# Kernel tuning notes

Measured on AMD Instinct MI355X. Metric: run time of the kernel, lower is better.

The kernel has to match this reference:

```python
import jax, jax.numpy as jnp
import numpy as np

EMBED_DIM = 1024
NUM_HEADS = 16
HEAD_DIM = EMBED_DIM // NUM_HEADS
EPSILON = 0.01
C = 2.0 + EPSILON
SCORE_SCALE = 1.0
B, L = 2, 2048


def setup_inputs() -> dict:
    key = jax.random.key(0)
    k0, k1, k2, k3, k4 = jax.random.split(key, 5)
    x = jax.random.normal(k0, (B, L, EMBED_DIM), dtype=jnp.float32)
    # flax Linear kernels: (in, out)
    W_qkv = jax.random.normal(k1, (EMBED_DIM, 3 * EMBED_DIM), dtype=jnp.float32) / np.sqrt(EMBED_DIM)
    b_qkv = jnp.zeros((3 * EMBED_DIM,), dtype=jnp.float32)
    W_out = jax.random.normal(k2, (EMBED_DIM, EMBED_DIM), dtype=jnp.float32) / np.sqrt(EMBED_DIM)
    b_out = jnp.zeros((EMBED_DIM,), dtype=jnp.float32)
    return {"x": x, "W_qkv": W_qkv, "b_qkv": b_qkv, "W_out": W_out, "b_out": b_out}


def reference(x, W_qkv, b_qkv, W_out, b_out):
    Bb, Ll, E = x.shape
    qkv = x @ W_qkv + b_qkv                      # [B, L, 3E]
    q, k, v = jnp.split(qkv, 3, axis=-1)
    def to_heads(t):
        return t.reshape(Bb, Ll, NUM_HEADS, HEAD_DIM).transpose(0, 2, 1, 3)  # [B,H,L,D]
    q, k, v = to_heads(q), to_heads(k), to_heads(v)
    q_norm = q / jnp.linalg.norm(q, axis=-1, keepdims=True)
    k_norm = k / jnp.linalg.norm(k, axis=-1, keepdims=True)
    x_dot = jnp.einsum('bhid,bhjd->bhij', q_norm, k_norm)   # [B,H,L,L]
    scores = (x_dot ** 2) / (C - 2.0 * x_dot) * SCORE_SCALE
    mask = jnp.triu(jnp.ones((Ll, Ll), dtype=scores.dtype), k=1) * -1e9
    scores = scores + mask[None, None, :, :]
    attn = jax.nn.softmax(scores, axis=-1)
    out = jnp.einsum('bhij,bhjd->bhid', attn, v)            # [B,H,L,D]
    out = out.transpose(0, 2, 1, 3).reshape(Bb, Ll, E)
    return out @ W_out + b_out
```

## Files before the change

kernel.cpp:

```cpp
#include <hip/hip_runtime.h>
#include <cstdint>
#include <cstddef>

#define B_DIM 2
#define L_DIM 2048
#define E_DIM 1024
#define H_DIM 16
#define HD    64
#define M_ROWS (B_DIM * L_DIM)
#define QKV_N  (3 * E_DIM)
#define C_CONST 2.01f
#define NCH_BH 40
#define LOG2E 1.4426950408889634f
#define LN2   0.6931471805599453f

typedef unsigned short ushort_t;
typedef __attribute__((ext_vector_type(8))) short bf16x8;
typedef __attribute__((ext_vector_type(4))) float f32x4;

__device__ __forceinline__ unsigned int f2bf(float f) {
    union { float f; unsigned int u; } v; v.f = f;
    return (v.u + 0x7FFFu + ((v.u >> 16) & 1u)) >> 16;
}
__device__ __forceinline__ float bf2f_lo(unsigned int u) {
    union { unsigned int u; float f; } v; v.u = u << 16; return v.f;
}
__device__ __forceinline__ float bf2f_hi(unsigned int u) {
    union { unsigned int u; float f; } v; v.u = u & 0xffff0000u; return v.f;
}

__device__ __forceinline__ void gload16(const void* g, void* l) {
    __builtin_amdgcn_global_load_lds(
        (const __attribute__((address_space(1))) void*)g,
        (__attribute__((address_space(3))) void*)l, 16, 0, 0);
}

__device__ __forceinline__ void transpose_tile_dev(
    const float* __restrict__ in, ushort_t* __restrict__ out,
    int R, int Cn, int c0, int r0, int tid, float t[64][65])
{
    for (int idx = tid; idx < 4096; idx += 256) {
        const int r = idx >> 6, c = idx & 63;
        t[r][c] = in[(size_t)(r0 + r) * Cn + c0 + c];
    }
    __syncthreads();
    for (int idx = tid; idx < 4096; idx += 256) {
        const int c = idx >> 6, r = idx & 63;
        out[(size_t)(c0 + c) * R + r0 + r] = (ushort_t)f2bf(t[r][c]);
    }
}

__global__ __launch_bounds__(256) void prep_kernel(
    const float* __restrict__ x, ushort_t* __restrict__ xb,
    const float* __restrict__ Wqkv, ushort_t* __restrict__ WqkvT,
    const float* __restrict__ Wout, ushort_t* __restrict__ WoutT)
{
    __shared__ float t[64][65];
    const int bx = blockIdx.x;
    const int tid = threadIdx.x;
    if (bx < 4096) {
        const int i = bx * 256 + tid;
        const float4 v = ((const float4*)x)[i];
        uint2 p;
        p.x = f2bf(v.x) | (f2bf(v.y) << 16);
        p.y = f2bf(v.z) | (f2bf(v.w) << 16);
        ((uint2*)xb)[i] = p;
    } else if (bx < 4096 + 768) {
        const int idx = bx - 4096;
        transpose_tile_dev(Wqkv, WqkvT, E_DIM, QKV_N, (idx % 48) * 64, (idx / 48) * 64, tid, t);
    } else {
        const int idx = bx - 4864;
        transpose_tile_dev(Wout, WoutT, E_DIM, E_DIM, (idx & 15) * 64, (idx >> 4) * 64, tid, t);
    }
}

template<int NCOLS, int MODE>
__global__ __launch_bounds__(256) void gemm_bt_kernel(
    const ushort_t* __restrict__ A, const ushort_t* __restrict__ BT,
    const float* __restrict__ bias, float* __restrict__ outf,
    ushort_t* __restrict__ q16, ushort_t* __restrict__ k16,
    ushort_t* __restrict__ vt16)
{
    __shared__ __align__(16) ushort_t Abuf[2][128 * 32];
    __shared__ __align__(16) ushort_t Bbuf[2][128 * 32];
    const int tid = threadIdx.x;
    const int wave = tid >> 6, lane = tid & 63;
    const int m0 = blockIdx.x * 128, n0 = blockIdx.y * 128;
    const int wr = (wave >> 1) * 64, wc = (wave & 1) * 64;
    const int g = lane >> 4, l15 = lane & 15;

    f32x4 acc[4][4];
    #pragma unroll
    for (int i = 0; i < 4; ++i)
        #pragma unroll
        for (int j = 0; j < 4; ++j) acc[i][j] = f32x4{0.f, 0.f, 0.f, 0.f};

    const int sr = tid >> 2;
    const int sc = (tid & 3) * 8;
    const ushort_t* Asrc0 = A + (size_t)(m0 + sr) * 1024 + sc;
    const ushort_t* Asrc1 = A + (size_t)(m0 + 64 + sr) * 1024 + sc;
    const ushort_t* Bsrc0 = BT + (size_t)(n0 + sr) * 1024 + sc;
    const ushort_t* Bsrc1 = BT + (size_t)(n0 + 64 + sr) * 1024 + sc;

    gload16(Asrc0, &Abuf[0][tid * 8]);
    gload16(Asrc1, &Abuf[0][2048 + tid * 8]);
    gload16(Bsrc0, &Bbuf[0][tid * 8]);
    gload16(Bsrc1, &Bbuf[0][2048 + tid * 8]);
    __syncthreads();

    for (int k0 = 0; k0 < 1024; k0 += 32) {
        const int cur = (k0 >> 5) & 1;
        if (k0 + 32 < 1024) {
            gload16(Asrc0 + k0 + 32, &Abuf[cur ^ 1][tid * 8]);
            gload16(Asrc1 + k0 + 32, &Abuf[cur ^ 1][2048 + tid * 8]);
            gload16(Bsrc0 + k0 + 32, &Bbuf[cur ^ 1][tid * 8]);
            gload16(Bsrc1 + k0 + 32, &Bbuf[cur ^ 1][2048 + tid * 8]);
        }

        bf16x8 af[4];
        #pragma unroll
        for (int mt = 0; mt < 4; ++mt)
            af[mt] = *(const bf16x8*)&Abuf[cur][(wr + mt * 16 + l15) * 32 + 8 * g];
        #pragma unroll
        for (int nt = 0; nt < 4; ++nt) {
            const bf16x8 bfr = *(const bf16x8*)&Bbuf[cur][(wc + nt * 16 + l15) * 32 + 8 * g];
            #pragma unroll
            for (int mt = 0; mt < 4; ++mt)
                acc[mt][nt] = __builtin_amdgcn_mfma_f32_16x16x32_bf16(af[mt], bfr, acc[mt][nt], 0, 0, 0);
        }
        __syncthreads();
    }

    if (MODE == 0) {
        const int nBase = n0 + wc;
        const int sel = nBase >> 10;
        const int h   = (nBase & 1023) >> 6;
        float bv[4];
        #pragma unroll
        for (int nt = 0; nt < 4; ++nt) bv[nt] = bias[nBase + nt * 16 + l15];

        if (sel <= 1) {
            ushort_t* dst16 = (sel == 0) ? q16 : k16;
            #pragma unroll
            for (int mt = 0; mt < 4; ++mt) {
                float val[4][4], ss[4] = {0.f, 0.f, 0.f, 0.f};
                #pragma unroll
                for (int nt = 0; nt < 4; ++nt)
                    #pragma unroll
                    for (int r = 0; r < 4; ++r) {
                        const float v = acc[mt][nt][r] + bv[nt];
                        val[nt][r] = v;
                        ss[r] = fmaf(v, v, ss[r]);
                    }
                #pragma unroll
                for (int r = 0; r < 4; ++r) {
                    float t = ss[r];
                    t += __shfl_xor(t, 1); t += __shfl_xor(t, 2);
                    t += __shfl_xor(t, 4); t += __shfl_xor(t, 8);
                    ss[r] = 1.0f / sqrtf(t);
                }
                #pragma unroll
                for (int r = 0; r < 4; ++r) {
                    const int m = m0 + wr + mt * 16 + 4 * g + r;
                    const int bb = m >> 11, ll = m & 2047;
                    ushort_t* base = dst16 + ((size_t)((bb * H_DIM + h) * L_DIM + ll)) * HD + l15;
                    #pragma unroll
                    for (int nt = 0; nt < 4; ++nt)
                        base[nt * 16] = (ushort_t)f2bf(val[nt][r] * ss[r]);
                }
            }
        } else {
            const int bb = m0 >> 11;
            #pragma unroll
            for (int nt = 0; nt < 4; ++nt) {
                const int d = nt * 16 + l15;
                ushort_t* vbase = vt16 + ((size_t)((bb * H_DIM + h) * HD + d)) * L_DIM;
                #pragma unroll
                for (int mt = 0; mt < 4; ++mt) {
                    const int key = (m0 & 2047) + wr + mt * 16 + 4 * g;
                    const float v0 = acc[mt][nt][0] + bv[nt];
                    const float v1 = acc[mt][nt][1] + bv[nt];
                    const float v2 = acc[mt][nt][2] + bv[nt];
                    const float v3 = acc[mt][nt][3] + bv[nt];
                    uint2 pk;
                    asm("v_cvt_pk_bf16_f32 %0, %1, %2" : "=v"(pk.x) : "v"(v0), "v"(v1));
                    asm("v_cvt_pk_bf16_f32 %0, %1, %2" : "=v"(pk.y) : "v"(v2), "v"(v3));
                    *(uint2*)&vbase[key] = pk;
                }
            }
        }
    } else {
        #pragma unroll
        for (int nt = 0; nt < 4; ++nt) {
            const int n = n0 + wc + nt * 16 + l15;
            const float bvv = bias[n];
            #pragma unroll
            for (int mt = 0; mt < 4; ++mt)
                #pragma unroll
                for (int r = 0; r < 4; ++r) {
                    const int m = m0 + wr + mt * 16 + 4 * g + r;
                    outf[(size_t)m * E_DIM + n] = acc[mt][nt][r] + bvv;
                }
        }
    }
}

__global__ __launch_bounds__(512) void attn_mfma_kernel(
    const ushort_t* __restrict__ qn, const ushort_t* __restrict__ kn,
    const ushort_t* __restrict__ vt,
    ushort_t* __restrict__ pO, float* __restrict__ pl, float* __restrict__ pm)
{
    __shared__ __align__(16) ushort_t Qs[128 * 64];
    __shared__ __align__(16) ushort_t Ks[2][64 * 64];
    __shared__ __align__(16) ushort_t Vs[2][64 * 64];

    int c = blockIdx.x, qtp = 0, s = 0;
    #pragma unroll
    for (int gg = 0; gg < 4; ++gg) {
        const int sz = 4 * (gg + 1);
        if (c < sz) { qtp = 4 * gg + c / (gg + 1); s = c - (c / (gg + 1)) * (gg + 1); break; }
        c -= sz;
    }
    const int bh = blockIdx.y;
    const int cid = bh * NCH_BH + blockIdx.x;
    const int q0 = qtp * 128;
    const int kt0 = 8 * s;
    const int ktEnd = min(8 * s + 8, 2 * qtp + 2);

    const int tid = threadIdx.x, w = tid >> 6, lane = tid & 63;
    const int g = lane >> 4, l15 = lane & 15;
    ushort_t* Pw = &Qs[w * 16 * 64];

    const ushort_t* Qg = qn + ((size_t)bh * L_DIM + q0) * HD;
    const ushort_t* Kg = kn + (size_t)bh * L_DIM * HD;
    const ushort_t* Vg = vt + (size_t)bh * HD * L_DIM;

    const int srow = tid >> 3, sch = tid & 7;
    const int qr2 = (tid + 512) >> 3, qc2 = (tid + 512) & 7;

    {
        const int j0 = kt0 * 64;
        gload16(Qg + srow * 64 + ((sch ^ (srow & 7)) << 3), Qs + srow * 64 + (sch << 3));
        gload16(Qg + qr2 * 64 + ((qc2 ^ (qr2 & 7)) << 3), Qs + qr2 * 64 + (qc2 << 3));
        gload16(Kg + (size_t)(j0 + srow) * 64 + ((sch ^ (srow & 7)) << 3), Ks[0] + srow * 64 + (sch << 3));
        gload16(Vg + (size_t)srow * L_DIM + j0 + ((sch ^ (srow & 7)) << 3), Vs[0] + srow * 64 + (sch << 3));
    }
    __syncthreads();

    bf16x8 qf[2];
    #pragma unroll
    for (int kc = 0; kc < 2; ++kc) {
        const int row = 16 * w + l15;
        qf[kc] = *(const bf16x8*)&Qs[row * 64 + (((4 * kc + g) ^ (row & 7)) << 3)];
    }

    f32x4 o[4];
    float M = 8.0f * LOG2E, l_i = 0.f;
    #pragma unroll
    for (int j = 0; j < 4; ++j) o[j] = f32x4{0.f, 0.f, 0.f, 0.f};

    const int qrow = q0 + 16 * w + l15;

    for (int kt = kt0; kt < ktEnd; ++kt) {
        const int cur = (kt - kt0) & 1;
        if (kt + 1 < ktEnd) {
            const int j1 = (kt + 1) * 64;
            gload16(Kg + (size_t)(j1 + srow) * 64 + ((sch ^ (srow & 7)) << 3),
                    Ks[cur ^ 1] + srow * 64 + (sch << 3));
            gload16(Vg + (size_t)srow * L_DIM + j1 + ((sch ^ (srow & 7)) << 3),
                    Vs[cur ^ 1] + srow * 64 + (sch << 3));
        }
        const int j0 = kt * 64;

        bf16x8 ak[4][2];
        #pragma unroll
        for (int kt4 = 0; kt4 < 4; ++kt4)
            #pragma unroll
            for (int kc = 0; kc < 2; ++kc) {
                const int row = 16 * kt4 + l15;
                ak[kt4][kc] = *(const bf16x8*)&Ks[cur][row * 64 + (((4 * kc + g) ^ (row & 7)) << 3)];
            }
        f32x4 st[4];
        #pragma unroll
        for (int kt4 = 0; kt4 < 4; ++kt4) st[kt4] = f32x4{0.f, 0.f, 0.f, 0.f};
        __builtin_amdgcn_s_setprio(1);
        #pragma unroll
        for (int kc = 0; kc < 2; ++kc)
            #pragma unroll
            for (int kt4 = 0; kt4 < 4; ++kt4)
                st[kt4] = __builtin_amdgcn_mfma_f32_16x16x32_bf16(
                    ak[kt4][kc], qf[kc], st[kt4], 0, 0, 0);
        __builtin_amdgcn_s_setprio(0);

        const float negM = -M;
        float emax = -1e30f;
        #pragma unroll
        for (int kt4 = 0; kt4 < 4; ++kt4)
            #pragma unroll
            for (int r = 0; r < 4; ++r) {
                const float x = st[kt4][r];
                const float t = (x * x) * LOG2E;
                const float d = fmaf(-2.f, x, C_CONST);
                float rr;
                asm("v_rcp_f32 %0, %1" : "=v"(rr) : "v"(d));
                const float e = fmaf(t, rr, negM);
                st[kt4][r] = e;
                emax = fmaxf(emax, e);
            }

        if (kt >= 2 * qtp) {
            emax = -1e30f;
            #pragma unroll
            for (int kt4 = 0; kt4 < 4; ++kt4)
                #pragma unroll
                for (int r = 0; r < 4; ++r) {
                    const int key = j0 + 16 * kt4 + 4 * g + r;
                    float e = st[kt4][r];
                    e = (key > qrow) ? -100.f : e;
                    st[kt4][r] = e;
                    emax = fmaxf(emax, e);
                }
        }

        if (__any(emax > 0.f)) {
            float rm = fmaxf(emax, __shfl_xor(emax, 16));
            rm = fmaxf(rm, __shfl_xor(rm, 32));
            rm = fmaxf(rm, 0.f);
            #pragma unroll
            for (int kt4 = 0; kt4 < 4; ++kt4)
                #pragma unroll
                for (int r = 0; r < 4; ++r) st[kt4][r] -= rm;
            const float nrm = -rm;
            float scl;
            asm("v_exp_f32 %0, %1" : "=v"(scl) : "v"(nrm));
            l_i *= scl;
            #pragma unroll
            for (int r = 0; r < 4; ++r) {
                const float sv = __shfl(scl, 4 * g + r);
                #pragma unroll
                for (int dt = 0; dt < 4; ++dt) o[dt][r] *= sv;
            }
            M += rm;
        }

        float ts = 0.f;
        #pragma unroll
        for (int kt4 = 0; kt4 < 4; ++kt4) {
            const float e0 = st[kt4][0], e1 = st[kt4][1];
            const float e2 = st[kt4][2], e3 = st[kt4][3];
            float p0, p1, p2, p3;
            asm("v_exp_f32 %0, %1" : "=v"(p0) : "v"(e0));
            asm("v_exp_f32 %0, %1" : "=v"(p1) : "v"(e1));
            asm("v_exp_f32 %0, %1" : "=v"(p2) : "v"(e2));
            asm("v_exp_f32 %0, %1" : "=v"(p3) : "v"(e3));
            ts += (p0 + p1) + (p2 + p3);
            uint2 pk;
            asm("v_cvt_pk_bf16_f32 %0, %1, %2" : "=v"(pk.x) : "v"(p0), "v"(p1));
            asm("v_cvt_pk_bf16_f32 %0, %1, %2" : "=v"(pk.y) : "v"(p2), "v"(p3));
            const int ch = 2 * kt4 + (g >> 1);
            *(uint2*)&Pw[l15 * 64 + ((ch ^ (l15 & 7)) << 3) + 4 * (g & 1)] = pk;
        }
        l_i += ts;

        bf16x8 ap[2], av[4][2];
        #pragma unroll
        for (int kc = 0; kc < 2; ++kc)
            ap[kc] = *(const bf16x8*)&Pw[l15 * 64 + (((4 * kc + g) ^ (l15 & 7)) << 3)];
        #pragma unroll
        for (int dt = 0; dt < 4; ++dt)
            #pragma unroll
            for (int kc = 0; kc < 2; ++kc) {
                const int row = 16 * dt + l15;
                av[dt][kc] = *(const bf16x8*)&Vs[cur][row * 64 + (((4 * kc + g) ^ (row & 7)) << 3)];
            }
        __builtin_amdgcn_s_setprio(1);
        #pragma unroll
        for (int kc = 0; kc < 2; ++kc)
            #pragma unroll
            for (int dt = 0; dt < 4; ++dt)
                o[dt] = __builtin_amdgcn_mfma_f32_16x16x32_bf16(
                    ap[kc], av[dt][kc], o[dt], 0, 0, 0);
        __builtin_amdgcn_s_setprio(0);

        __syncthreads();
    }

    l_i += __shfl_xor(l_i, 16);
    l_i += __shfl_xor(l_i, 32);
    ushort_t* po = pO + (size_t)cid * 8192 + (16 * w) * 64;
    #pragma unroll
    for (int r = 0; r < 4; ++r)
        #pragma unroll
        for (int dt = 0; dt < 4; ++dt)
            po[(4 * g + r) * 64 + 16 * dt + l15] = (ushort_t)f2bf(o[dt][r]);
    if (lane < 16) {
        pl[cid * 128 + 16 * w + lane] = l_i;
        pm[cid * 128 + 16 * w + lane] = M * LN2;
    }
}

__global__ __launch_bounds__(256) void combine_kernel(
    const ushort_t* __restrict__ pO, const float* __restrict__ pl,
    const float* __restrict__ pm, ushort_t* __restrict__ cb)
{
    const int qt2 = blockIdx.x, bh = blockIdx.y;
    const int qtp = qt2 >> 1, half = qt2 & 1;
    const int gg = qtp >> 2, ns = gg + 1;
    const int cid0 = bh * NCH_BH + 2 * gg * (gg + 1) + (qtp & 3) * ns;
    const int tid = threadIdx.x;
    const int row = tid >> 2, seg = tid & 3;
    const int rowc = half * 64 + row;

    float mt = -1e30f;
    for (int s2 = 0; s2 < ns; ++s2)
        mt = fmaxf(mt, pm[(cid0 + s2) * 128 + rowc]);

    float acc[16];
    #pragma unroll
    for (int j = 0; j < 16; ++j) acc[j] = 0.f;
    float l_tot = 0.f;
    for (int s2 = 0; s2 < ns; ++s2) {
        const int cid = cid0 + s2;
        const float sc = __expf(pm[cid * 128 + rowc] - mt);
        l_tot += pl[cid * 128 + rowc] * sc;
        const ushort_t* src = pO + (size_t)cid * 8192 + rowc * 64 + seg * 16;
        const uint4 u0 = *(const uint4*)src;
        const uint4 u1 = *(const uint4*)(src + 8);
        const unsigned int uu[8] = {u0.x, u0.y, u0.z, u0.w, u1.x, u1.y, u1.z, u1.w};
        #pragma unroll
        for (int j = 0; j < 8; ++j) {
            acc[2 * j]     = fmaf(sc, bf2f_lo(uu[j]), acc[2 * j]);
            acc[2 * j + 1] = fmaf(sc, bf2f_hi(uu[j]), acc[2 * j + 1]);
        }
    }
    const float inv = 1.0f / l_tot;
    const int b = bh >> 4, h = bh & 15;
    ushort_t* dst = cb + ((size_t)(b * L_DIM + qt2 * 64 + row)) * E_DIM + h * HD + seg * 16;
    uint4 w0, w1;
    w0.x = f2bf(acc[0] * inv)  | (f2bf(acc[1] * inv) << 16);
    w0.y = f2bf(acc[2] * inv)  | (f2bf(acc[3] * inv) << 16);
    w0.z = f2bf(acc[4] * inv)  | (f2bf(acc[5] * inv) << 16);
    w0.w = f2bf(acc[6] * inv)  | (f2bf(acc[7] * inv) << 16);
    w1.x = f2bf(acc[8] * inv)  | (f2bf(acc[9] * inv) << 16);
    w1.y = f2bf(acc[10] * inv) | (f2bf(acc[11] * inv) << 16);
    w1.z = f2bf(acc[12] * inv) | (f2bf(acc[13] * inv) << 16);
    w1.w = f2bf(acc[14] * inv) | (f2bf(acc[15] * inv) << 16);
    *(uint4*)dst = w0;
    *(uint4*)(dst + 8) = w1;
}

extern "C" void kernel_launch(void* const* d_in, const int* in_sizes, int n_in,
                              void* d_out, int out_size, void* d_ws, size_t ws_size,
                              hipStream_t stream)
{
    const float* x    = (const float*)d_in[0];
    const float* Wqkv = (const float*)d_in[1];
    const float* bqkv = (const float*)d_in[2];
    const float* Wout = (const float*)d_in[3];
    const float* bout = (const float*)d_in[4];
    float* out = (float*)d_out;

    char* ws = (char*)d_ws;
    const size_t MB = 1u << 20;
    ushort_t* qn16  = (ushort_t*)(ws + 0 * MB);
    ushort_t* kn16  = (ushort_t*)(ws + 8 * MB);
    ushort_t* vt16  = (ushort_t*)(ws + 24 * MB);
    ushort_t* xb    = (ushort_t*)(ws + 32 * MB);
    ushort_t* cb    = (ushort_t*)(ws + 32 * MB);
    ushort_t* WqkvT = (ushort_t*)(ws + 40 * MB);
    ushort_t* pO    = (ushort_t*)(ws + 40 * MB);
    float*    pl    = (float*)   (ws + 60 * MB);
    float*    pm    = (float*)   (ws + 61 * MB);
    ushort_t* WoutT = (ushort_t*)(ws + 62 * MB);

    prep_kernel<<<5120, 256, 0, stream>>>(x, xb, Wqkv, WqkvT, Wout, WoutT);

    gemm_bt_kernel<QKV_N, 0><<<dim3(M_ROWS / 128, QKV_N / 128), 256, 0, stream>>>(
        xb, WqkvT, bqkv, nullptr, qn16, kn16, vt16);

    attn_mfma_kernel<<<dim3(NCH_BH, B_DIM * H_DIM), 512, 0, stream>>>(qn16, kn16, vt16, pO, pl, pm);

    combine_kernel<<<dim3(L_DIM / 64, B_DIM * H_DIM), 256, 0, stream>>>(pO, pl, pm, cb);

    gemm_bt_kernel<E_DIM, 1><<<dim3(M_ROWS / 128, E_DIM / 128), 256, 0, stream>>>(
        cb, WoutT, bout, out, nullptr, nullptr, nullptr);
}
```

Baseline: 133.3 us.

## Use K=64 single-buffered GEMM tiles with XOR-swizzled LDS layout

The projection GEMM now stages 64-wide K slices into a single LDS buffer instead of double-buffered 32-wide slices. The global-to-LDS loads use an XOR swizzle of 16-byte chunks by row, which is meant to cut LDS bank conflicts on the fragment reads, and each barrier pair now covers twice as many MFMAs. The cost is losing the prefetch overlap, since loads and compute are now serialized by two barriers per iteration.

```diff
diff --git a/kernel.cpp b/kernel.cpp
--- a/kernel.cpp
+++ b/kernel.cpp
@@ -81,8 +81,8 @@
     ushort_t* __restrict__ q16, ushort_t* __restrict__ k16,
     ushort_t* __restrict__ vt16)
 {
-    __shared__ __align__(16) ushort_t Abuf[2][128 * 32];
-    __shared__ __align__(16) ushort_t Bbuf[2][128 * 32];
+    __shared__ __align__(16) ushort_t Abuf[128 * 64];
+    __shared__ __align__(16) ushort_t Bbuf[128 * 64];
     const int tid = threadIdx.x;
     const int wave = tid >> 6, lane = tid & 63;
     const int m0 = blockIdx.x * 128, n0 = blockIdx.y * 128;
@@ -95,40 +95,39 @@
         #pragma unroll
         for (int j = 0; j < 4; ++j) acc[i][j] = f32x4{0.f, 0.f, 0.f, 0.f};
 
-    const int sr = tid >> 2;
-    const int sc = (tid & 3) * 8;
-    const ushort_t* Asrc0 = A + (size_t)(m0 + sr) * 1024 + sc;
-    const ushort_t* Asrc1 = A + (size_t)(m0 + 64 + sr) * 1024 + sc;
-    const ushort_t* Bsrc0 = BT + (size_t)(n0 + sr) * 1024 + sc;
-    const ushort_t* Bsrc1 = BT + (size_t)(n0 + 64 + sr) * 1024 + sc;
-
-    gload16(Asrc0, &Abuf[0][tid * 8]);
-    gload16(Asrc1, &Abuf[0][2048 + tid * 8]);
-    gload16(Bsrc0, &Bbuf[0][tid * 8]);
-    gload16(Bsrc1, &Bbuf[0][2048 + tid * 8]);
-    __syncthreads();
-
-    for (int k0 = 0; k0 < 1024; k0 += 32) {
-        const int cur = (k0 >> 5) & 1;
-        if (k0 + 32 < 1024) {
-            gload16(Asrc0 + k0 + 32, &Abuf[cur ^ 1][tid * 8]);
-            gload16(Asrc1 + k0 + 32, &Abuf[cur ^ 1][2048 + tid * 8]);
-            gload16(Bsrc0 + k0 + 32, &Bbuf[cur ^ 1][tid * 8]);
-            gload16(Bsrc1 + k0 + 32, &Bbuf[cur ^ 1][2048 + tid * 8]);
-        }
-
-        bf16x8 af[4];
+    const ushort_t* Asrc = A + (size_t)m0 * 1024;
+    const ushort_t* Bsrc = BT + (size_t)n0 * 1024;
+
+    for (int k0 = 0; k0 < 1024; k0 += 64) {
+        __syncthreads();
+        #pragma unroll
+        for (int p = 0; p < 4; ++p) {
+            const int cidx = tid + 256 * p;
+            const int row = cidx >> 3, ch = cidx & 7;
+            const int soff = ((ch ^ (row & 7)) << 3);
+            gload16(Asrc + (size_t)row * 1024 + k0 + soff, &Abuf[row * 64 + (ch << 3)]);
+            gload16(Bsrc + (size_t)row * 1024 + k0 + soff, &Bbuf[row * 64 + (ch << 3)]);
+        }
+        __syncthreads();
+
+        bf16x8 af[4][2];
         #pragma unroll
         for (int mt = 0; mt < 4; ++mt)
-            af[mt] = *(const bf16x8*)&Abuf[cur][(wr + mt * 16 + l15) * 32 + 8 * g];
-        #pragma unroll
-        for (int nt = 0; nt < 4; ++nt) {
-            const bf16x8 bfr = *(const bf16x8*)&Bbuf[cur][(wc + nt * 16 + l15) * 32 + 8 * g];
-            #pragma unroll
-            for (int mt = 0; mt < 4; ++mt)
-                acc[mt][nt] = __builtin_amdgcn_mfma_f32_16x16x32_bf16(af[mt], bfr, acc[mt][nt], 0, 0, 0);
-        }
-        __syncthreads();
+            #pragma unroll
+            for (int kc = 0; kc < 2; ++kc) {
+                const int row = wr + mt * 16 + l15;
+                af[mt][kc] = *(const bf16x8*)&Abuf[row * 64 + (((g + 4 * kc) ^ (row & 7)) << 3)];
+            }
+        #pragma unroll
+        for (int kc = 0; kc < 2; ++kc)
+            #pragma unroll
+            for (int nt = 0; nt < 4; ++nt) {
+                const int row = wc + nt * 16 + l15;
+                const bf16x8 bfr = *(const bf16x8*)&Bbuf[row * 64 + (((g + 4 * kc) ^ (row & 7)) << 3)];
+                #pragma unroll
+                for (int mt = 0; mt < 4; ++mt)
+                    acc[mt][nt] = __builtin_amdgcn_mfma_f32_16x16x32_bf16(af[mt][kc], bfr, acc[mt][nt], 0, 0, 0);
+            }
     }
 
     if (MODE == 0) {
```

Result: faster. 129.7 us (-2.7%).
